# Kernel tuning notes

Hardware: AMD Instinct MI355X
Metric: run time of the kernel (lower is better)

Reference implementation:

```python
import jax, jax.numpy as jnp
import numpy as np

ALPHA = 0.4  # LeakyReLU negative slope used by the GAT


def _gat_head(h, W, a):
    # h: [N, F], W: [F, Fp], a: [2*Fp]; adjacency is all-ones so no masking
    Wh = h @ W                                   # [N, Fp]
    Fp = W.shape[1]
    e = jax.nn.leaky_relu(Wh @ a[:Fp][:, None] + (Wh @ a[Fp:])[None, :], ALPHA)
    att = jax.nn.softmax(e, axis=-1)             # [N, N]
    return att @ Wh                              # [N, Fp]


def _gat(h, W_heads, a_heads, W_gout, a_gout):
    # multi-head GAT: concat elu(head outputs), then single output attention layer
    heads = jax.vmap(_gat_head, in_axes=(None, 0, 0))(h, W_heads, a_heads)  # [H, N, Fp]
    x = jax.nn.elu(heads).transpose(1, 0, 2).reshape(h.shape[0], -1)        # [N, H*Fp]
    return jax.nn.elu(_gat_head(x, W_gout, a_gout))                          # [N, Cg]


def setup_inputs() -> dict:
    key = jax.random.key(0)
    ks = jax.random.split(key, 20)
    bs, R, S = 4, 512, 54
    h, w = 100, 152
    fc_dim, convs_dim4 = 1024, 512
    Cg, H, So = 256, 4, 128
    Fp = Cg // H
    sc = lambda k, shp, s=0.05: jax.random.normal(k, shp, dtype=jnp.float32) * s
    return {
        'region_f': jax.random.normal(ks[0], (bs * R, fc_dim), dtype=jnp.float32),
        'stuff_f': jax.random.normal(ks[1], (bs, convs_dim4, h, w), dtype=jnp.float32),
        'semseg_score': jax.random.normal(ks[2], (bs, S, h, w), dtype=jnp.float32),
        'W_rin': sc(ks[3], (fc_dim, Cg)), 'b_rin': jnp.zeros((Cg,), jnp.float32),
        'W_sin': sc(ks[4], (convs_dim4, Cg)), 'b_sin': jnp.zeros((Cg,), jnp.float32),
        'W_heads': sc(ks[5], (H, Cg, Fp), 0.1), 'a_heads': sc(ks[6], (H, 2 * Fp), 0.1),
        'W_gout': sc(ks[7], (H * Fp, Cg), 0.1), 'a_gout': sc(ks[8], (2 * Cg,), 0.1),
        'W_rout': sc(ks[9], (Cg, Cg)), 'b_rout': jnp.zeros((Cg,), jnp.float32),
        'W_sout': sc(ks[10], (Cg, So)), 'b_sout': jnp.zeros((So,), jnp.float32),
        'W_seg': sc(ks[11], (convs_dim4 + So, S)), 'b_seg': jnp.zeros((S,), jnp.float32),
    }


def reference(region_f, stuff_f, semseg_score,
              W_rin, b_rin, W_sin, b_sin,
              W_heads, a_heads, W_gout, a_gout,
              W_rout, b_rout, W_sout, b_sout,
              W_seg, b_seg):
    bs, Cd, h, w = stuff_f.shape
    S = semseg_score.shape[1]
    R = region_f.shape[0] // bs
    Cg = W_rin.shape[1]

    # node construction
    region_nodes = region_f @ W_rin + b_rin                           # [bs*R, Cg]
    score_flat = semseg_score.reshape(bs, S, h * w)
    class_center = jnp.einsum('bsn,bcn->bsc',
                              jax.nn.softmax(score_flat, axis=-1),
                              stuff_f.reshape(bs, Cd, h * w))          # [bs, S, Cd]
    class_nodes = class_center @ W_sin + b_sin                         # [bs, S, Cg]

    # per-image dense GAT over region + stuff nodes (batched via vmap)
    nodes = jnp.concatenate([region_nodes.reshape(bs, R, Cg), class_nodes], axis=1)
    graph_nodes = jax.vmap(lambda x: _gat(x, W_heads, a_heads, W_gout, a_gout))(nodes)
    new_region, new_class = graph_nodes[:, :R], graph_nodes[:, R:]

    # new box features: concat of original region features and projected graph features
    new_region_f = jnp.concatenate(
        [region_f, new_region.reshape(bs * R, Cg) @ W_rout + b_rout], axis=-1)

    # new stuff features: scatter class nodes back to pixels via class softmax
    new_class_nodes = new_class @ W_sout + b_sout                      # [bs, S, So]
    attn = jax.nn.softmax(score_flat, axis=1)                          # softmax over classes
    new_stuff = jnp.einsum('bsn,bso->bon', attn, new_class_nodes)      # [bs, So, h*w]
    new_stuff = new_stuff.reshape(bs, -1, h, w)

    # 1x1 conv seg head + x4 bilinear upsample (align_corners=False)
    seg_in = jnp.concatenate([stuff_f, new_stuff], axis=1)
    seg = jnp.einsum('bchw,co->bohw', seg_in, W_seg) + b_seg[None, :, None, None]
    segments = jax.image.resize(seg, (bs, S, 4 * h, 4 * w), method='bilinear')
    return new_region_f, segments
```

## Files before the change

kernel.cpp:

```cpp
#include <hip/hip_runtime.h>

#define HW 15200
#define SSD 54
#define NBATCH 4
#define NNODE 566
#define NPAD 576
#define CGD 256
#define CDD 512
#define NSPLIT 25
#define KSPAN 608

typedef __attribute__((ext_vector_type(4))) float f32x4;
typedef __attribute__((ext_vector_type(8))) short bf16x8;
typedef unsigned short ushort_t;

#define BT_RIN   0
#define BT_SIN   262144
#define BT_HEADS 393216
#define BT_GOUT  458752
#define BT_ROUT  524288
#define BT_SOUT  589824
#define BT_SEG2  622592
#define BT_TOTAL 630784

static constexpr long OFF_P     = 0;
static constexpr long OFF_CC    = OFF_P     + (long)NBATCH*SSD*HW;
static constexpr long OFF_NODES = OFF_CC    + (long)NBATCH*64*CDD;
static constexpr long OFF_WH    = OFF_NODES + (long)NBATCH*NNODE*CGD;
static constexpr long OFF_S1    = OFF_WH    + (long)16*NNODE*64;
static constexpr long OFF_S2    = OFF_S1    + 16*NPAD;
static constexpr long OFF_X     = OFF_S2    + 16*NPAD;
static constexpr long OFF_WH2   = OFF_X     + (long)NBATCH*NNODE*CGD;
static constexpr long OFF_S1B   = OFF_WH2   + (long)NBATCH*NNODE*CGD;
static constexpr long OFF_S2B   = OFF_S1B   + NBATCH*NPAD;
static constexpr long OFF_G     = OFF_S2B   + NBATCH*NPAD;
static constexpr long OFF_SUMS  = OFF_G     + (long)NBATCH*NNODE*CGD;
static constexpr long OFF_BT    = OFF_SUMS  + 256;
static constexpr long OFF_ASEG  = OFF_BT    + (BT_TOTAL/2 + 8);
static constexpr long OFF_SEG   = OFF_ASEG  + (long)NBATCH*64*576/2;
static constexpr long OFF_RFB   = OFF_SEG   + (long)NBATCH*SSD*HW;
static constexpr long OFF_WCOMB = OFF_RFB   + 1048576;
static constexpr long OFF_B2    = OFF_WCOMB + 8192;
static constexpr long OFF_ATTNB = OFF_B2    + 64;

__device__ inline float lrelu04(float x){ return x >= 0.f ? x : 0.4f*x; }
__device__ inline float eluf(float x){ return x > 0.f ? x : __expf(x) - 1.f; }
__device__ inline ushort_t f2bf(float f){
    unsigned u = __float_as_uint(f);
    return (ushort_t)((u + 0x7FFFu + ((u >> 16) & 1u)) >> 16);
}
__device__ inline float bf2f(ushort_t u){ return __uint_as_float((unsigned)u << 16); }
__device__ inline bf16x8 pack8(float4 lo, float4 hi){
    union { bf16x8 v; ushort_t u[8]; } p;
    p.u[0]=f2bf(lo.x); p.u[1]=f2bf(lo.y); p.u[2]=f2bf(lo.z); p.u[3]=f2bf(lo.w);
    p.u[4]=f2bf(hi.x); p.u[5]=f2bf(hi.y); p.u[6]=f2bf(hi.z); p.u[7]=f2bf(hi.w);
    return p.v;
}

__global__ __launch_bounds__(512)
void softmax_p(const float* __restrict__ score, ushort_t* __restrict__ pb,
               float* __restrict__ sums, float* __restrict__ s1s2b_zero,
               float* __restrict__ ccp)
{
    int blk = blockIdx.x;
    int t = threadIdx.x;
    if (blk < 256) {
        int b = blk >> 6, s = blk & 63;
        ushort_t* prow = pb + ((long)b*64 + s)*HW;
        if (s >= SSD) {
            for (int i = t; i < HW; i += 512) prow[i] = 0;
            if (t == 0) sums[b*64 + s] = 1.f;
            return;
        }
        const float* row = score + ((long)b*SSD + s)*HW;
        __shared__ float red[8];
        float s_ = 0.f;
        for (int i = t; i < HW; i += 512) {
            float e = __expf(row[i]);
            s_ += e;
            prow[i] = f2bf(e);
        }
        #pragma unroll
        for (int off = 32; off >= 1; off >>= 1) s_ += __shfl_down(s_, off);
        if ((t & 63) == 0) red[t >> 6] = s_;
        __syncthreads();
        if (t == 0) {
            float tot = 0.f;
            #pragma unroll
            for (int u = 0; u < 8; ++u) tot += red[u];
            sums[b*64 + s] = tot;
        }
        return;
    }
    long gid = (long)(blk - 256)*512 + t;
    if (gid < 4608) { s1s2b_zero[gid] = 0.f; return; }
    gid -= 4608;
    if (gid < (long)NBATCH*64*CDD) ccp[gid] = 0.f;
}

__global__ __launch_bounds__(256)
void cc_prep(const ushort_t* __restrict__ pb, const float* __restrict__ stuff,
             ushort_t* __restrict__ sbout, float* __restrict__ ccp,
             const float* __restrict__ score, ushort_t* __restrict__ attnb,
             const float* __restrict__ rf, float* __restrict__ out_region,
             ushort_t* __restrict__ rfb,
             const float* __restrict__ W_seg, ushort_t* __restrict__ asegb,
             const float* __restrict__ W_rin, const float* __restrict__ W_sin,
             const float* __restrict__ W_heads, const float* __restrict__ W_gout,
             const float* __restrict__ W_rout, const float* __restrict__ W_sout,
             const float* __restrict__ b_sout,
             ushort_t* __restrict__ bt, ushort_t* __restrict__ wcomb,
             float* __restrict__ bias2)
{
    int bid = blockIdx.x;
    if (bid < 832) {
        int g = (bid >> 6) * 8 + (bid & 7);
        if (g >= NSPLIT*NBATCH) return;
        int nt = (bid >> 3) & 7;
        int ks = g >> 2, b = g & 3;

        int w = threadIdx.x >> 6, l = threadIdx.x & 63;
        int lr = l & 15, lk = l >> 4;
        int n0 = nt*64 + w*16;
        const ushort_t* Prow = pb + ((long)b*64 + lr)*HW;
        const float*    Srow = stuff + ((long)b*CDD + n0 + lr)*HW;
        ushort_t*       Sout = sbout + ((long)b*CDD + n0 + lr)*HW;
        f32x4 acc[4] = {};
        int kbeg = ks * KSPAN;
        for (int k0 = kbeg; k0 < kbeg + KSPAN; k0 += 32) {
            int kk = k0 + lk*8;
            float4 lo = *(const float4*)&Srow[kk];
            float4 hi = *(const float4*)&Srow[kk + 4];
            bf16x8 bfv = pack8(lo, hi);
            *(bf16x8*)&Sout[kk] = bfv;
            #pragma unroll
            for (int mi = 0; mi < 4; ++mi) {
                bf16x8 af = *(const bf16x8*)&Prow[(long)mi*16*HW + kk];
                acc[mi] = __builtin_amdgcn_mfma_f32_16x16x32_bf16(af, bfv, acc[mi], 0, 0, 0);
            }
        }
        int c = n0 + lr;
        #pragma unroll
        for (int mi = 0; mi < 4; ++mi)
            #pragma unroll
            for (int r = 0; r < 4; ++r) {
                int m = mi*16 + lk*4 + r;
                atomicAdd(&ccp[((long)b*64 + m)*CDD + c], acc[mi][r]);
            }
        return;
    }
    long gid = (long)(bid - 832) * 256 + threadIdx.x;
    if (gid < (long)NBATCH*HW) {
        int b = (int)(gid / HW), n = (int)(gid % HW);
        const float* sp = score + (long)b*SSD*HW + n;
        float v[SSD];
        float m = -1e30f;
        #pragma unroll
        for (int s = 0; s < SSD; ++s) { v[s] = sp[(long)s*HW]; m = fmaxf(m, v[s]); }
        float sum = 0.f;
        #pragma unroll
        for (int s = 0; s < SSD; ++s) { v[s] = __expf(v[s] - m); sum += v[s]; }
        float inv = 1.f / sum;
        ushort_t* ap = attnb + (long)b*64*HW + n;
        #pragma unroll
        for (int s = 0; s < SSD; ++s) ap[(long)s*HW] = f2bf(v[s] * inv);
        #pragma unroll
        for (int s = SSD; s < 64; ++s) ap[(long)s*HW] = 0;
        return;
    }
    gid -= (long)NBATCH*HW;
    if (gid < 524288) {
        long row = gid / 256, col = gid % 256;
        float4 v = reinterpret_cast<const float4*>(rf)[gid];
        reinterpret_cast<float4*>(out_region)[row*320 + col] = v;
        union { ushort_t u[4]; uint2 q; } pk;
        pk.u[0]=f2bf(v.x); pk.u[1]=f2bf(v.y); pk.u[2]=f2bf(v.z); pk.u[3]=f2bf(v.w);
        reinterpret_cast<uint2*>(rfb)[gid] = pk.q;
        return;
    }
    gid -= 524288;
    if (gid < 131072) {
        int b = (int)(gid >> 15);
        int r = (int)(gid & 32767);
        int o = r >> 9, k = r & 511;
        asegb[(long)b*36864 + (long)o*576 + k] = f2bf(o < SSD ? W_seg[k*SSD + o] : 0.f);
        return;
    }
    gid -= 131072;
    if (gid < BT_TOTAL) {
        int i = (int)gid;
        float v;
        if (i < BT_SIN)        { int j=i;            int n=j>>10, k=j&1023; v = W_rin[k*256+n]; }
        else if (i < BT_HEADS) { int j=i-BT_SIN;     int n=j>>9,  k=j&511;  v = W_sin[k*256+n]; }
        else if (i < BT_GOUT)  { int j=i-BT_HEADS;   int h=j>>14, r=j&16383; int f=r>>8, k=r&255;
                                 v = W_heads[(h*256+k)*64+f]; }
        else if (i < BT_ROUT)  { int j=i-BT_GOUT;    int n=j>>8,  k=j&255;  v = W_gout[k*256+n]; }
        else if (i < BT_SOUT)  { int j=i-BT_ROUT;    int n=j>>8,  k=j&255;  v = W_rout[k*256+n]; }
        else if (i < BT_SEG2)  { int j=i-BT_SOUT;    int n=j>>8,  k=j&255;  v = W_sout[k*128+n]; }
        else                   { int j=i-BT_SEG2;    int o=j>>7,  k=j&127;
                                 v = (o < SSD) ? W_seg[(512+k)*SSD + o] : 0.f; }
        bt[i] = f2bf(v);
        return;
    }
    gid -= BT_TOTAL;
    if (gid < 16384) {
        int od = (int)(gid >> 8), k = (int)(gid & 255);
        float v = 0.f;
        if (od < SSD)
            for (int o = 0; o < 128; ++o)
                v += W_sout[k*128 + o] * W_seg[(512+o)*SSD + od];
        wcomb[(long)od*256 + k] = f2bf(v);
        return;
    }
    gid -= 16384;
    if (gid < 64) {
        int od = (int)gid;
        float v = 0.f;
        if (od < SSD)
            for (int o = 0; o < 128; ++o)
                v += b_sout[o] * W_seg[(512+o)*SSD + od];
        bias2[od] = v;
    }
}

__device__ __forceinline__
void seg512_body(int nt, int b,
                 const ushort_t* __restrict__ stuffb,
                 const ushort_t* __restrict__ asegb, const float* __restrict__ b_seg,
                 float* __restrict__ seg)
{
    int w = threadIdx.x >> 6, l = threadIdx.x & 63;
    int lr = l & 15, lk = l >> 4;
    int n0 = nt*128 + w*32;
    const ushort_t* A = asegb + (long)b*36864;
    const ushort_t* S = stuffb + (long)b*CDD*HW;
    f32x4 acc[4][2] = {};
    int n1 = min(n0 + lr, HW-1);
    int n2 = min(n0 + 16 + lr, HW-1);

    for (int k0 = 0; k0 < 512; k0 += 32) {
        const ushort_t* Bsrc = S + (long)k0*HW;
        long kb = (long)(lk*8)*HW;
        union { bf16x8 v; ushort_t u[8]; } b0, b1;
        #pragma unroll
        for (int u = 0; u < 8; ++u) {
            b0.u[u] = Bsrc[kb + (long)u*HW + n1];
            b1.u[u] = Bsrc[kb + (long)u*HW + n2];
        }
        #pragma unroll
        for (int ot = 0; ot < 4; ++ot) {
            bf16x8 af = *(const bf16x8*)&A[(ot*16 + lr)*576 + k0 + lk*8];
            acc[ot][0] = __builtin_amdgcn_mfma_f32_16x16x32_bf16(af, b0.v, acc[ot][0], 0,0,0);
            acc[ot][1] = __builtin_amdgcn_mfma_f32_16x16x32_bf16(af, b1.v, acc[ot][1], 0,0,0);
        }
    }

    #pragma unroll
    for (int ot = 0; ot < 4; ++ot) {
        #pragma unroll
        for (int r = 0; r < 4; ++r) {
            int o = ot*16 + lk*4 + r;
            if (o >= SSD) continue;
            float bb = b_seg[o];
            int na = n0 + lr, nb = n0 + 16 + lr;
            if (na < HW) seg[((long)b*SSD + o)*HW + na] = acc[ot][0][r] + bb;
            if (nb < HW) seg[((long)b*SSD + o)*HW + nb] = acc[ot][1][r] + bb;
        }
    }
}

__device__ __forceinline__
void segk64_body(int nt, int b,
                 const ushort_t* __restrict__ attnb,
                 const ushort_t* __restrict__ asegb,
                 float* __restrict__ seg)
{
    int w = threadIdx.x >> 6, l = threadIdx.x & 63;
    int lr = l & 15, lk = l >> 4;
    int n0 = nt*128 + w*32;
    const ushort_t* A = asegb + (long)b*36864;
    const ushort_t* T = attnb + (long)b*64*HW;
    f32x4 acc[4][2] = {};
    int n1 = min(n0 + lr, HW-1);
    int n2 = min(n0 + 16 + lr, HW-1);

    #pragma unroll
    for (int k0 = 512; k0 < 576; k0 += 32) {
        const ushort_t* Bsrc = T + (long)(k0-512)*HW;
        long kb = (long)(lk*8)*HW;
        union { bf16x8 v; ushort_t u[8]; } b0, b1;
        #pragma unroll
        for (int u = 0; u < 8; ++u) {
            b0.u[u] = Bsrc[kb + (long)u*HW + n1];
            b1.u[u] = Bsrc[kb + (long)u*HW + n2];
        }
        #pragma unroll
        for (int ot = 0; ot < 4; ++ot) {
            bf16x8 af = *(const bf16x8*)&A[(ot*16 + lr)*576 + k0 + lk*8];
            acc[ot][0] = __builtin_amdgcn_mfma_f32_16x16x32_bf16(af, b0.v, acc[ot][0], 0,0,0);
            acc[ot][1] = __builtin_amdgcn_mfma_f32_16x16x32_bf16(af, b1.v, acc[ot][1], 0,0,0);
        }
    }

    #pragma unroll
    for (int ot = 0; ot < 4; ++ot) {
        #pragma unroll
        for (int r = 0; r < 4; ++r) {
            int o = ot*16 + lk*4 + r;
            if (o >= SSD) continue;
            int na = n0 + lr, nb = n0 + 16 + lr;
            if (na < HW) { long i = ((long)b*SSD + o)*HW + na; seg[i] += acc[ot][0][r]; }
            if (nb < HW) { long i = ((long)b*SSD + o)*HW + nb; seg[i] += acc[ot][1][r]; }
        }
    }
}

template<bool AF32, int OUTMODE>
__device__ __forceinline__
void mm_body(int bx, int by, int bz,
             const void* __restrict__ Ap, const ushort_t* __restrict__ Bt,
             void* __restrict__ Cp, const float* __restrict__ bias,
             int M, int N, int K, int lda, int ldc,
             long sA, int zdivA, long sB, int zmodB, long sC)
{
    int z = bz;
    int w = threadIdx.x >> 6, l = threadIdx.x & 63;
    int lr = l & 15, lk = l >> 4;
    int m0 = bx * 64 + w * 16;
    int n0 = by * 64;
    const ushort_t* bt = Bt + (long)(z % zmodB) * sB;
    int mload = min(m0 + lr, M - 1);
    const float*    Af = (const float*)Ap    + (long)(z / zdivA) * sA + (long)mload * lda;
    const ushort_t* Ab = (const ushort_t*)Ap + (long)(z / zdivA) * sA + (long)mload * lda;
    f32x4 acc[4] = {};

    #pragma unroll 2
    for (int k0 = 0; k0 < K; k0 += 32) {
        int kk = k0 + lk * 8;
        bf16x8 af;
        if (AF32) {
            float4 lo = *(const float4*)&Af[kk];
            float4 hi = *(const float4*)&Af[kk + 4];
            af = pack8(lo, hi);
        } else {
            af = *(const bf16x8*)&Ab[kk];
        }
        #pragma unroll
        for (int j = 0; j < 4; ++j) {
            bf16x8 bf = *(const bf16x8*)&bt[(long)(n0 + j*16 + lr) * K + kk];
            acc[j] = __builtin_amdgcn_mfma_f32_16x16x32_bf16(af, bf, acc[j], 0, 0, 0);
        }
    }

    #pragma unroll
    for (int j = 0; j < 4; ++j) {
        int n = n0 + j*16 + lr;
        float bb = bias ? bias[n] : 0.f;
        #pragma unroll
        for (int r = 0; r < 4; ++r) {
            int m = m0 + lk*4 + r;
            if (OUTMODE == 2) {
                float v = acc[j][r] + bb;
                ((ushort_t*)Cp)[(long)z * sC + (long)n * ldc + m] =
                    (m < M) ? f2bf(v) : (ushort_t)0;
            } else {
                if (m >= M) continue;
                float v = acc[j][r] + bb;
                if (OUTMODE == 0)
                    ((float*)Cp)[(long)z * sC + (long)m * ldc + n] = v;
                else
                    ((ushort_t*)Cp)[(long)z * sC + (long)m * ldc + n] = f2bf(v);
            }
        }
    }
}

__global__ __launch_bounds__(256)
void nodes_seg(const ushort_t* __restrict__ rfb, const ushort_t* __restrict__ btRin,
               const float* __restrict__ ccp, const float* __restrict__ sums,
               const ushort_t* __restrict__ btSin, ushort_t* __restrict__ nodes,
               const float* __restrict__ b_rin, const float* __restrict__ b_sin,
               const ushort_t* __restrict__ stuffb, const ushort_t* __restrict__ asegb,
               const float* __restrict__ b_seg, float* __restrict__ segb)
{
    int bid = blockIdx.x;
    if (bid >= 144) {
        int sid = bid - 144;
        seg512_body(sid % 119, sid / 119, stuffb, asegb, b_seg, segb);
        return;
    }
    int bx = bid % 9, by = (bid/9) % 4, bz = bid / 36;
    if (bx < 8) {
        mm_body<false, 1>(bx, by, bz, rfb, btRin, nodes, b_rin,
                          512, 256, 1024, 1024, 256, 512L*1024, 1, 0, 1, (long)NNODE*CGD);
        return;
    }
    int w = threadIdx.x >> 6, l = threadIdx.x & 63;
    int lr = l & 15, lk = l >> 4;
    int m0 = w * 16, n0 = by * 64;
    int mload = min(m0 + lr, SSD - 1);
    const float* Af = ccp + ((long)bz*64 + mload)*CDD;
    float inv = 1.f / sums[bz*64 + mload];
    f32x4 acc[4] = {};

    #pragma unroll 2
    for (int k0 = 0; k0 < CDD; k0 += 32) {
        int kk = k0 + lk * 8;
        float4 lo = *(const float4*)&Af[kk];
        float4 hi = *(const float4*)&Af[kk + 4];
        lo.x *= inv; lo.y *= inv; lo.z *= inv; lo.w *= inv;
        hi.x *= inv; hi.y *= inv; hi.z *= inv; hi.w *= inv;
        bf16x8 af = pack8(lo, hi);
        #pragma unroll
        for (int j = 0; j < 4; ++j) {
            bf16x8 bf = *(const bf16x8*)&btSin[(long)(n0 + j*16 + lr) * CDD + kk];
            acc[j] = __builtin_amdgcn_mfma_f32_16x16x32_bf16(af, bf, acc[j], 0, 0, 0);
        }
    }

    #pragma unroll
    for (int j = 0; j < 4; ++j) {
        int n = n0 + j*16 + lr;
        float bb = b_sin[n];
        #pragma unroll
        for (int r = 0; r < 4; ++r) {
            int m = m0 + lk*4 + r;
            if (m >= SSD) continue;
            nodes[(long)bz*NNODE*CGD + (long)(512 + m)*CGD + n] = f2bf(acc[j][r] + bb);
        }
    }
}

__global__ __launch_bounds__(256)
void wht_seg(const ushort_t* __restrict__ nodes, const ushort_t* __restrict__ btHeads,
             ushort_t* __restrict__ wht, const float* __restrict__ a_heads,
             float* __restrict__ s1, float* __restrict__ s2,
             const ushort_t* __restrict__ stuffb, const ushort_t* __restrict__ asegb,
             const float* __restrict__ b_seg, float* __restrict__ segb)
{
    int bid = blockIdx.x;
    if (bid >= 144) {
        int sid = bid - 144 + 80;
        seg512_body(sid % 119, sid / 119, stuffb, asegb, b_seg, segb);
        return;
    }
    int bx = bid % 9, z = bid / 9;
    int w = threadIdx.x >> 6, l = threadIdx.x & 63;
    int lr = l & 15, lk = l >> 4;
    int m0 = bx*64 + w*16;
    const ushort_t* bt = btHeads + (long)(z & 3) * (64L*256);
    int mload = min(m0 + lr, NNODE - 1);
    const ushort_t* Ab = nodes + (long)(z >> 2)*((long)NNODE*CGD) + (long)mload*CGD;
    f32x4 acc[4] = {};

    #pragma unroll 2
    for (int k0 = 0; k0 < 256; k0 += 32) {
        int kk = k0 + lk*8;
        bf16x8 af = *(const bf16x8*)&Ab[kk];
        #pragma unroll
        for (int j = 0; j < 4; ++j) {
            bf16x8 bf = *(const bf16x8*)&bt[(long)(j*16 + lr)*256 + kk];
            acc[j] = __builtin_amdgcn_mfma_f32_16x16x32_bf16(af, bf, acc[j], 0, 0, 0);
        }
    }

    const float* av = a_heads + (long)(z & 3)*128;
    ushort_t* Wout = wht + (long)z*(64L*NPAD);
    float p1[4] = {0.f,0.f,0.f,0.f}, p2[4] = {0.f,0.f,0.f,0.f};
    #pragma unroll
    for (int j = 0; j < 4; ++j) {
        int f = j*16 + lr;
        float c1 = av[f], c2 = av[64 + f];
        #pragma unroll
        for (int r = 0; r < 4; ++r) {
            int m = m0 + lk*4 + r;
            float v = acc[j][r];
            Wout[(long)f*NPAD + m] = (m < NNODE) ? f2bf(v) : (ushort_t)0;
            if (m < NNODE) { p1[r] += v*c1; p2[r] += v*c2; }
        }
    }
    #pragma unroll
    for (int r = 0; r < 4; ++r)
        #pragma unroll
        for (int off = 1; off < 16; off <<= 1) {
            p1[r] += __shfl_xor(p1[r], off);
            p2[r] += __shfl_xor(p2[r], off);
        }
    if (lr == 0) {
        #pragma unroll
        for (int r = 0; r < 4; ++r) {
            int m = m0 + lk*4 + r;
            if (m < NNODE) {
                s1[(long)z*NPAD + m] = p1[r];
                s2[(long)z*NPAD + m] = p2[r];
            }
        }
    }
}

template<int F, int HEADMODE>
__device__ __forceinline__
void att_body(int bx, int z, const ushort_t* __restrict__ WhTall,
              const float* __restrict__ s1v, const float* __restrict__ s2v,
              ushort_t* __restrict__ outbuf)
{
    constexpr int FT = F / 16;
    const ushort_t* W  = WhTall + (long)z * F * NPAD;
    const float* s1 = s1v + (long)z * NPAD;
    const float* s2 = s2v + (long)z * NPAD;
    int w = threadIdx.x >> 6, l = threadIdx.x & 63;
    int lr = l & 15, lk = l >> 4;

    __shared__ float s2sh[NPAD];
    __shared__ float redm[4];
    float mxl = -1e30f;
    for (int i = threadIdx.x; i < NPAD; i += 256) {
        float v = (i < NNODE) ? s2[i] : -1e30f;
        s2sh[i] = v;
        mxl = fmaxf(mxl, v);
    }
    #pragma unroll
    for (int off = 32; off >= 1; off >>= 1) mxl = fmaxf(mxl, __shfl_down(mxl, off));
    if (l == 0) redm[w] = mxl;
    __syncthreads();
    float s2max = fmaxf(fmaxf(redm[0], redm[1]), fmaxf(redm[2], redm[3]));

    int m0 = bx * 64 + w * 16;
    float s1r = s1[min(m0 + lr, NNODE - 1)];
    float mrow = lrelu04(s1r + s2max);

    union { bf16x8 v; ushort_t u[8]; } onesu;
    #pragma unroll
    for (int u = 0; u < 8; ++u) onesu.u[u] = 0x3F80;
    bf16x8 ones = onesu.v;

    f32x4 acc[FT] = {};
    f32x4 accw = {};

    for (int j0 = 0; j0 < NPAD; j0 += 32) {
        float wv[8];
        #pragma unroll
        for (int u = 0; u < 8; ++u) {
            float e = lrelu04(s1r + s2sh[j0 + lk*8 + u]);
            wv[u] = __expf(e - mrow);
        }
        float4 lo = {wv[0], wv[1], wv[2], wv[3]};
        float4 hi = {wv[4], wv[5], wv[6], wv[7]};
        bf16x8 af = pack8(lo, hi);
        accw = __builtin_amdgcn_mfma_f32_16x16x32_bf16(af, ones, accw, 0, 0, 0);
        #pragma unroll
        for (int ft = 0; ft < FT; ++ft) {
            bf16x8 bf = *(const bf16x8*)&W[(long)(ft*16 + lr)*NPAD + j0 + lk*8];
            acc[ft] = __builtin_amdgcn_mfma_f32_16x16x32_bf16(af, bf, acc[ft], 0, 0, 0);
        }
    }

    #pragma unroll
    for (int r = 0; r < 4; ++r) {
        int m = m0 + lk*4 + r;
        if (m >= NNODE) continue;
        float inv = 1.f / accw[r];
        #pragma unroll
        for (int ft = 0; ft < FT; ++ft) {
            int f = ft*16 + lr;
            float v = eluf(acc[ft][r] * inv);
            if (HEADMODE) {
                int b = z >> 2, h = z & 3;
                outbuf[((long)(b*NNODE + m))*CGD + h*64 + f] = f2bf(v);
            } else {
                outbuf[((long)(z*NNODE + m))*CGD + f] = f2bf(v);
            }
        }
    }
}

__global__ __launch_bounds__(256)
void att64_seg(const ushort_t* __restrict__ wht, const float* __restrict__ s1,
               const float* __restrict__ s2, ushort_t* __restrict__ xbuf,
               const ushort_t* __restrict__ stuffb, const ushort_t* __restrict__ asegb,
               const float* __restrict__ b_seg, float* __restrict__ segb)
{
    int bid = blockIdx.x;
    if (bid >= 144) {
        int sid = bid - 144 + 160;
        seg512_body(sid % 119, sid / 119, stuffb, asegb, b_seg, segb);
        return;
    }
    att_body<64, 1>(bid % 9, bid / 9, wht, s1, s2, xbuf);
}

__global__ __launch_bounds__(256)
void wht2_seg(const ushort_t* __restrict__ xbuf, const ushort_t* __restrict__ btGout,
              ushort_t* __restrict__ wht2, const float* __restrict__ a_gout,
              float* __restrict__ s1b, float* __restrict__ s2b,
              const ushort_t* __restrict__ stuffb, const ushort_t* __restrict__ asegb,
              const float* __restrict__ b_seg, float* __restrict__ segb)
{
    int bid = blockIdx.x;
    if (bid >= 144) {
        int sid = bid - 144 + 240;
        seg512_body(sid % 119, sid / 119, stuffb, asegb, b_seg, segb);
        return;
    }
    int bx = bid % 9, by = (bid/9) % 4, z = bid / 36;
    int w = threadIdx.x >> 6, l = threadIdx.x & 63;
    int lr = l & 15, lk = l >> 4;
    int m0 = bx*64 + w*16;
    int n0 = by*64;
    int mload = min(m0 + lr, NNODE - 1);
    const ushort_t* Ab = xbuf + (long)z*((long)NNODE*CGD) + (long)mload*CGD;
    f32x4 acc[4] = {};

    #pragma unroll 2
    for (int k0 = 0; k0 < 256; k0 += 32) {
        int kk = k0 + lk*8;
        bf16x8 af = *(const bf16x8*)&Ab[kk];
        #pragma unroll
        for (int j = 0; j < 4; ++j) {
            bf16x8 bf = *(const bf16x8*)&btGout[(long)(n0 + j*16 + lr)*256 + kk];
            acc[j] = __builtin_amdgcn_mfma_f32_16x16x32_bf16(af, bf, acc[j], 0, 0, 0);
        }
    }

    ushort_t* Wout = wht2 + (long)z*(256L*NPAD);
    float p1[4] = {0.f,0.f,0.f,0.f}, p2[4] = {0.f,0.f,0.f,0.f};
    #pragma unroll
    for (int j = 0; j < 4; ++j) {
        int f = n0 + j*16 + lr;
        float c1 = a_gout[f], c2 = a_gout[256 + f];
        #pragma unroll
        for (int r = 0; r < 4; ++r) {
            int m = m0 + lk*4 + r;
            float v = acc[j][r];
            Wout[(long)f*NPAD + m] = (m < NNODE) ? f2bf(v) : (ushort_t)0;
            if (m < NNODE) { p1[r] += v*c1; p2[r] += v*c2; }
        }
    }
    #pragma unroll
    for (int r = 0; r < 4; ++r)
        #pragma unroll
        for (int off = 1; off < 16; off <<= 1) {
            p1[r] += __shfl_xor(p1[r], off);
            p2[r] += __shfl_xor(p2[r], off);
        }
    if (lr == 0) {
        #pragma unroll
        for (int r = 0; r < 4; ++r) {
            int m = m0 + lk*4 + r;
            if (m < NNODE) {
                atomicAdd(&s1b[(long)z*NPAD + m], p1[r]);
                atomicAdd(&s2b[(long)z*NPAD + m], p2[r]);
            }
        }
    }
}

__global__ __launch_bounds__(256)
void attg_seg(const ushort_t* __restrict__ wht2, const float* __restrict__ s1v,
              const float* __restrict__ s2v, ushort_t* __restrict__ g,
              const ushort_t* __restrict__ wcomb, const float* __restrict__ bias2,
              ushort_t* __restrict__ asegm2,
              const ushort_t* __restrict__ stuffb, const ushort_t* __restrict__ asegb,
              const float* __restrict__ b_seg, float* __restrict__ segb)
{
    int bid = blockIdx.x;
    if (bid >= 36) {
        int sid = bid - 36 + 320;
        seg512_body(sid % 119, sid / 119, stuffb, asegb, b_seg, segb);
        return;
    }
    int bx = bid % 9, z = bid / 9;
    const ushort_t* W  = wht2 + (long)z * (256L*NPAD);
    const float* s1 = s1v + (long)z * NPAD;
    const float* s2 = s2v + (long)z * NPAD;
    int t = threadIdx.x;
    int w = t >> 6, l = t & 63;
    int lr = l & 15, lk = l >> 4;

    __shared__ float s2sh[NPAD];
    __shared__ float redm[4];
    __shared__ ushort_t gld[64][264];

    float mxl = -1e30f;
    for (int i = t; i < NPAD; i += 256) {
        float v = (i < NNODE) ? s2[i] : -1e30f;
        s2sh[i] = v;
        mxl = fmaxf(mxl, v);
    }
    if (bx == 8)
        for (int i = t; i < 10*264; i += 256) gld[54 + i/264][i%264] = 0;
    #pragma unroll
    for (int off = 32; off >= 1; off >>= 1) mxl = fmaxf(mxl, __shfl_down(mxl, off));
    if (l == 0) redm[w] = mxl;
    __syncthreads();
    float s2max = fmaxf(fmaxf(redm[0], redm[1]), fmaxf(redm[2], redm[3]));

    int m0 = bx * 64 + w * 16;
    float s1r = s1[min(m0 + lr, NNODE - 1)];
    float mrow = lrelu04(s1r + s2max);

    union { bf16x8 v; ushort_t u[8]; } onesu;
    #pragma unroll
    for (int u = 0; u < 8; ++u) onesu.u[u] = 0x3F80;
    bf16x8 ones = onesu.v;

    f32x4 acc[16] = {};
    f32x4 accw = {};

    for (int j0 = 0; j0 < NPAD; j0 += 32) {
        float wv[8];
        #pragma unroll
        for (int u = 0; u < 8; ++u) {
            float e = lrelu04(s1r + s2sh[j0 + lk*8 + u]);
            wv[u] = __expf(e - mrow);
        }
        float4 lo = {wv[0], wv[1], wv[2], wv[3]};
        float4 hi = {wv[4], wv[5], wv[6], wv[7]};
        bf16x8 af = pack8(lo, hi);
        accw = __builtin_amdgcn_mfma_f32_16x16x32_bf16(af, ones, accw, 0, 0, 0);
        #pragma unroll
        for (int ft = 0; ft < 16; ++ft) {
            bf16x8 bf = *(const bf16x8*)&W[(long)(ft*16 + lr)*NPAD + j0 + lk*8];
            acc[ft] = __builtin_amdgcn_mfma_f32_16x16x32_bf16(af, bf, acc[ft], 0, 0, 0);
        }
    }

    #pragma unroll
    for (int r = 0; r < 4; ++r) {
        int m = m0 + lk*4 + r;
        if (m >= NNODE) continue;
        float inv = 1.f / accw[r];
        #pragma unroll
        for (int ft = 0; ft < 16; ++ft) {
            int f = ft*16 + lr;
            ushort_t vb = f2bf(eluf(acc[ft][r] * inv));
            g[((long)(z*NNODE + m))*CGD + f] = vb;
            if (bx == 8) gld[m - 512][f] = vb;
        }
    }

    if (bx == 8) {
        __syncthreads();
        f32x4 acc2[4] = {};
        #pragma unroll 2
        for (int k0 = 0; k0 < 256; k0 += 32) {
            int kk = k0 + lk*8;
            bf16x8 af = *(const bf16x8*)&gld[w*16 + lr][kk];
            #pragma unroll
            for (int j = 0; j < 4; ++j) {
                bf16x8 bf = *(const bf16x8*)&wcomb[(long)(j*16 + lr)*256 + kk];
                acc2[j] = __builtin_amdgcn_mfma_f32_16x16x32_bf16(af, bf, acc2[j], 0, 0, 0);
            }
        }
        #pragma unroll
        for (int j = 0; j < 4; ++j) {
            int n = j*16 + lr;
            float bb = bias2[n];
            #pragma unroll
            for (int r = 0; r < 4; ++r) {
                int m = w*16 + lk*4 + r;
                asegm2[(long)z*36864 + (long)n*576 + m] =
                    (m < SSD) ? f2bf(acc2[j][r] + bb) : (ushort_t)0;
            }
        }
    }
}

__global__ __launch_bounds__(256)
void rout_segk(const ushort_t* __restrict__ g_bf, const ushort_t* __restrict__ btRout,
               float* __restrict__ outreg, const float* __restrict__ b_rout,
               const ushort_t* __restrict__ attnb, const ushort_t* __restrict__ asegb,
               float* __restrict__ segb)
{
    int bid = blockIdx.x;
    if (bid < 128) {
        int x = bid & 7, y = (bid >> 3) & 3, z = bid >> 5;
        mm_body<false, 0>(x, y, z, g_bf, btRout, outreg, b_rout,
                          512, 256, 256, 256, 1280, (long)NNODE*CGD, 1, 0, 1, 512L*1280);
    } else {
        int sid = bid - 128;
        segk64_body(sid % 119, sid / 119, attnb, asegb, segb);
    }
}

__global__ __launch_bounds__(256)
void resize_v2_kernel(const float* __restrict__ seg, float* __restrict__ out)
{
    long u = (long)blockIdx.x * 256 + threadIdx.x;
    const long TOT4 = (long)NBATCH * SSD * 400 * 152;
    if (u >= TOT4) return;
    int m = (int)(u % 152);
    long r = u / 152;
    int y = (int)(r % 400);
    long c = r / 400;
    float fy = y * 0.25f - 0.375f;
    int y0 = (int)floorf(fy);
    float wy = fy - (float)y0;
    int y0c = max(y0, 0), y1c = min(y0 + 1, 99);
    const float* sp = seg + c * HW;
    int xm = max(m - 1, 0), xp = min(m + 1, 151);
    float r0a = sp[y0c * 152 + xm], r0b = sp[y0c * 152 + m], r0c = sp[y0c * 152 + xp];
    float r1a = sp[y1c * 152 + xm], r1b = sp[y1c * 152 + m], r1c = sp[y1c * 152 + xp];
    float ra = r0a + wy * (r1a - r0a);
    float rb = r0b + wy * (r1b - r0b);
    float rc = r0c + wy * (r1c - r0c);
    float4 o4;
    o4.x = 0.375f * ra + 0.625f * rb;
    o4.y = 0.125f * ra + 0.875f * rb;
    o4.z = 0.875f * rb + 0.125f * rc;
    o4.w = 0.625f * rb + 0.375f * rc;
    reinterpret_cast<float4*>(out)[u] = o4;
}

extern "C" void kernel_launch(void* const* d_in, const int* in_sizes, int n_in,
                              void* d_out, int out_size, void* d_ws, size_t ws_size,
                              hipStream_t stream)
{
    const float* region_f = (const float*)d_in[0];
    const float* stuff    = (const float*)d_in[1];
    const float* score    = (const float*)d_in[2];
    const float* W_rin    = (const float*)d_in[3];
    const float* b_rin    = (const float*)d_in[4];
    const float* W_sin    = (const float*)d_in[5];
    const float* b_sin    = (const float*)d_in[6];
    const float* W_heads  = (const float*)d_in[7];
    const float* a_heads  = (const float*)d_in[8];
    const float* W_gout   = (const float*)d_in[9];
    const float* a_gout   = (const float*)d_in[10];
    const float* W_rout   = (const float*)d_in[11];
    const float* b_rout   = (const float*)d_in[12];
    const float* W_sout   = (const float*)d_in[13];
    const float* b_sout   = (const float*)d_in[14];
    const float* W_seg    = (const float*)d_in[15];
    const float* b_seg    = (const float*)d_in[16];

    float* out = (float*)d_out;
    float* ws  = (float*)d_ws;

    ushort_t* pb   = (ushort_t*)(ws + OFF_P);
    float* ccp     = ws + OFF_CC;
    ushort_t* nodes_bf = (ushort_t*)(ws + OFF_NODES);
    ushort_t* wht  = (ushort_t*)(ws + OFF_WH);
    float* s1      = ws + OFF_S1;
    float* s2      = ws + OFF_S2;
    ushort_t* xbuf_bf = (ushort_t*)(ws + OFF_X);
    ushort_t* wht2 = (ushort_t*)(ws + OFF_WH2);
    float* s1b     = ws + OFF_S1B;
    float* s2b     = ws + OFF_S2B;
    ushort_t* g_bf = (ushort_t*)(ws + OFF_G);
    float* sums    = ws + OFF_SUMS;
    ushort_t* bt   = (ushort_t*)(ws + OFF_BT);
    ushort_t* asegb = (ushort_t*)(ws + OFF_ASEG);
    float* segb    = ws + OFF_SEG;
    ushort_t* rfb  = (ushort_t*)(ws + OFF_RFB);
    ushort_t* wcomb = (ushort_t*)(ws + OFF_WCOMB);
    float* bias2v  = ws + OFF_B2;
    ushort_t* attnb = (ushort_t*)(ws + OFF_ATTNB);

    float* out_region = out;
    float* out_seg    = out + 2048L*1280;
    ushort_t* stuffb  = (ushort_t*)out_seg;

    softmax_p<<<521, 512, 0, stream>>>(score, pb, sums, s1b, ccp);

    cc_prep<<<6158, 256, 0, stream>>>(pb, stuff, stuffb, ccp, score, attnb,
                                      region_f, out_region, rfb, W_seg, asegb,
                                      W_rin, W_sin, W_heads, W_gout, W_rout, W_sout,
                                      b_sout, bt, wcomb, bias2v);

    nodes_seg<<<224, 256, 0, stream>>>(
        rfb, bt + BT_RIN, ccp, sums, bt + BT_SIN, nodes_bf, b_rin, b_sin,
        stuffb, asegb, b_seg, segb);

    wht_seg<<<224, 256, 0, stream>>>(
        nodes_bf, bt + BT_HEADS, wht, a_heads, s1, s2,
        stuffb, asegb, b_seg, segb);

    att64_seg<<<224, 256, 0, stream>>>(
        wht, s1, s2, xbuf_bf, stuffb, asegb, b_seg, segb);

    wht2_seg<<<224, 256, 0, stream>>>(
        xbuf_bf, bt + BT_GOUT, wht2, a_gout, s1b, s2b,
        stuffb, asegb, b_seg, segb);

    attg_seg<<<192, 256, 0, stream>>>(
        wht2, s1b, s2b, g_bf, wcomb, bias2v, asegb + 512,
        stuffb, asegb, b_seg, segb);

    rout_segk<<<604, 256, 0, stream>>>(
        g_bf, bt + BT_ROUT, out_region + 1024, b_rout, attnb, asegb, segb);

    resize_v2_kernel<<<((long)NBATCH*SSD*400*152 + 255)/256, 256, 0, stream>>>(segb, out_seg);
}
```

Measured before the change: 282.7 us.

## Fuse score exponentiation and row sums into cc_prep, dropping softmax_p buffer

Removes the separate softmax_p kernel, which wrote exp(score) as a bf16 buffer plus row sums. cc_prep now computes exp(score) on the fly inside its MFMA loop and accumulates the row sums with atomics, and a small zero_init kernel clears the accumulators. This saves one full write and read of the intermediate buffer. In exchange, each fp32 score element is re-read and re-exponentiated by many waves, and padded class rows now keep a zero sum instead of one, which risks a divide-by-zero downstream.

```diff
diff --git a/kernel.cpp b/kernel.cpp
--- a/kernel.cpp
+++ b/kernel.cpp
@@ -57,50 +57,22 @@
     return p.v;
 }
 
-__global__ __launch_bounds__(512)
-void softmax_p(const float* __restrict__ score, ushort_t* __restrict__ pb,
-               float* __restrict__ sums, float* __restrict__ s1s2b_zero,
-               float* __restrict__ ccp)
-{
-    int blk = blockIdx.x;
-    int t = threadIdx.x;
-    if (blk < 256) {
-        int b = blk >> 6, s = blk & 63;
-        ushort_t* prow = pb + ((long)b*64 + s)*HW;
-        if (s >= SSD) {
-            for (int i = t; i < HW; i += 512) prow[i] = 0;
-            if (t == 0) sums[b*64 + s] = 1.f;
-            return;
-        }
-        const float* row = score + ((long)b*SSD + s)*HW;
-        __shared__ float red[8];
-        float s_ = 0.f;
-        for (int i = t; i < HW; i += 512) {
-            float e = __expf(row[i]);
-            s_ += e;
-            prow[i] = f2bf(e);
-        }
-        #pragma unroll
-        for (int off = 32; off >= 1; off >>= 1) s_ += __shfl_down(s_, off);
-        if ((t & 63) == 0) red[t >> 6] = s_;
-        __syncthreads();
-        if (t == 0) {
-            float tot = 0.f;
-            #pragma unroll
-            for (int u = 0; u < 8; ++u) tot += red[u];
-            sums[b*64 + s] = tot;
-        }
-        return;
-    }
-    long gid = (long)(blk - 256)*512 + t;
-    if (gid < 4608) { s1s2b_zero[gid] = 0.f; return; }
-    gid -= 4608;
-    if (gid < (long)NBATCH*64*CDD) ccp[gid] = 0.f;
-}
-
 __global__ __launch_bounds__(256)
-void cc_prep(const ushort_t* __restrict__ pb, const float* __restrict__ stuff,
+void zero_init(float* __restrict__ ccp, float* __restrict__ s1s2b,
+               float* __restrict__ sums)
+{
+    long i = (long)blockIdx.x*256 + threadIdx.x;
+    if (i < (long)NBATCH*64*CDD) { ccp[i] = 0.f; return; }
+    i -= (long)NBATCH*64*CDD;
+    if (i < 2L*NBATCH*NPAD) { s1s2b[i] = 0.f; return; }
+    i -= 2L*NBATCH*NPAD;
+    if (i < 256) sums[i] = 0.f;
+}
+
+__global__ __launch_bounds__(256)
+void cc_prep(const float* __restrict__ stuff,
              ushort_t* __restrict__ sbout, float* __restrict__ ccp,
+             float* __restrict__ sums,
              const float* __restrict__ score, ushort_t* __restrict__ attnb,
              const float* __restrict__ rf, float* __restrict__ out_region,
              ushort_t* __restrict__ rfb,
@@ -122,10 +94,10 @@
         int w = threadIdx.x >> 6, l = threadIdx.x & 63;
         int lr = l & 15, lk = l >> 4;
         int n0 = nt*64 + w*16;
-        const ushort_t* Prow = pb + ((long)b*64 + lr)*HW;
-        const float*    Srow = stuff + ((long)b*CDD + n0 + lr)*HW;
-        ushort_t*       Sout = sbout + ((long)b*CDD + n0 + lr)*HW;
+        const float* Srow = stuff + ((long)b*CDD + n0 + lr)*HW;
+        ushort_t*    Sout = sbout + ((long)b*CDD + n0 + lr)*HW;
         f32x4 acc[4] = {};
+        float rsum[4] = {0.f, 0.f, 0.f, 0.f};
         int kbeg = ks * KSPAN;
         for (int k0 = kbeg; k0 < kbeg + KSPAN; k0 += 32) {
             int kk = k0 + lk*8;
@@ -135,7 +107,19 @@
             *(bf16x8*)&Sout[kk] = bfv;
             #pragma unroll
             for (int mi = 0; mi < 4; ++mi) {
-                bf16x8 af = *(const bf16x8*)&Prow[(long)mi*16*HW + kk];
+                int s = lr + mi*16;
+                bf16x8 af = {};
+                if (s < SSD) {
+                    const float* sc = score + ((long)b*SSD + s)*HW + kk;
+                    float4 a0 = *(const float4*)sc;
+                    float4 a1 = *(const float4*)(sc + 4);
+                    a0.x = __expf(a0.x); a0.y = __expf(a0.y);
+                    a0.z = __expf(a0.z); a0.w = __expf(a0.w);
+                    a1.x = __expf(a1.x); a1.y = __expf(a1.y);
+                    a1.z = __expf(a1.z); a1.w = __expf(a1.w);
+                    rsum[mi] += a0.x + a0.y + a0.z + a0.w + a1.x + a1.y + a1.z + a1.w;
+                    af = pack8(a0, a1);
+                }
                 acc[mi] = __builtin_amdgcn_mfma_f32_16x16x32_bf16(af, bfv, acc[mi], 0, 0, 0);
             }
         }
@@ -147,6 +131,16 @@
                 int m = mi*16 + lk*4 + r;
                 atomicAdd(&ccp[((long)b*64 + m)*CDD + c], acc[mi][r]);
             }
+        if (nt == 0 && w == 0) {
+            #pragma unroll
+            for (int mi = 0; mi < 4; ++mi) {
+                float v = rsum[mi];
+                v += __shfl_down(v, 16);
+                v += __shfl_down(v, 32);
+                int s = lr + mi*16;
+                if (lk == 0 && s < SSD) atomicAdd(&sums[b*64 + s], v);
+            }
+        }
         return;
     }
     long gid = (long)(bid - 832) * 256 + threadIdx.x;
@@ -837,7 +831,6 @@
     float* out = (float*)d_out;
     float* ws  = (float*)d_ws;
 
-    ushort_t* pb   = (ushort_t*)(ws + OFF_P);
     float* ccp     = ws + OFF_CC;
     ushort_t* nodes_bf = (ushort_t*)(ws + OFF_NODES);
     ushort_t* wht  = (ushort_t*)(ws + OFF_WH);
@@ -861,9 +854,9 @@
     float* out_seg    = out + 2048L*1280;
     ushort_t* stuffb  = (ushort_t*)out_seg;
 
-    softmax_p<<<521, 512, 0, stream>>>(score, pb, sums, s1b, ccp);
-
-    cc_prep<<<6158, 256, 0, stream>>>(pb, stuff, stuffb, ccp, score, attnb,
+    zero_init<<<532, 256, 0, stream>>>(ccp, s1b, sums);
+
+    cc_prep<<<6158, 256, 0, stream>>>(stuff, stuffb, ccp, sums, score, attnb,
                                       region_f, out_region, rfb, W_seg, asegb,
                                       W_rin, W_sin, W_heads, W_gout, W_rout, W_sout,
                                       b_sout, bt, wcomb, bias2v);
```

New measurement: 280.9 us. Within noise of the previous version (-0.6%).

## Split fp32→bf16 stuff conversion from class-context GEMM and widen K-split

Applied to the files above, without the earlier changes.

The stuff-feature bf16 conversion now runs as an elementwise streaming pass inside a merged prep kernel, which also takes over the softmax, the zeroing and the weight prep. The class-context GEMM becomes a separate kernel that reads the bf16 copy, with the K-split raised from 25 to 95 chunks so far more blocks are in flight. The softmax loops are vectorised to float4 loads and 8-wide zero stores. In exchange, the stuff tensor is now read twice (once as fp32, once as bf16), and the wider split means more atomicAdd traffic on the accumulation buffer.

```diff
diff --git a/kernel.cpp b/kernel.cpp
--- a/kernel.cpp
+++ b/kernel.cpp
@@ -7,8 +7,10 @@
 #define NPAD 576
 #define CGD 256
 #define CDD 512
-#define NSPLIT 25
-#define KSPAN 608
+#define NSPLIT 95
+#define KSPAN 160
+#define NGRP (NSPLIT*NBATCH)
+#define CCBLK 3072
 
 typedef __attribute__((ext_vector_type(4))) float f32x4;
 typedef __attribute__((ext_vector_type(8))) short bf16x8;
@@ -57,10 +59,22 @@
     return p.v;
 }
 
-__global__ __launch_bounds__(512)
-void softmax_p(const float* __restrict__ score, ushort_t* __restrict__ pb,
-               float* __restrict__ sums, float* __restrict__ s1s2b_zero,
-               float* __restrict__ ccp)
+#define SB_GIDS 1945600L
+__global__ __launch_bounds__(256)
+void stream_prep(const float* __restrict__ score, ushort_t* __restrict__ pb,
+                 float* __restrict__ sums,
+                 const float* __restrict__ stuff, ushort_t* __restrict__ stuffb,
+                 ushort_t* __restrict__ attnb,
+                 const float* __restrict__ rf, float* __restrict__ out_region,
+                 ushort_t* __restrict__ rfb,
+                 const float* __restrict__ W_seg, ushort_t* __restrict__ asegb,
+                 const float* __restrict__ W_rin, const float* __restrict__ W_sin,
+                 const float* __restrict__ W_heads, const float* __restrict__ W_gout,
+                 const float* __restrict__ W_rout, const float* __restrict__ W_sout,
+                 const float* __restrict__ b_sout,
+                 ushort_t* __restrict__ bt, ushort_t* __restrict__ wcomb,
+                 float* __restrict__ bias2,
+                 float* __restrict__ ccp, float* __restrict__ s1s2b)
 {
     int blk = blockIdx.x;
     int t = threadIdx.x;
@@ -68,88 +82,44 @@
         int b = blk >> 6, s = blk & 63;
         ushort_t* prow = pb + ((long)b*64 + s)*HW;
         if (s >= SSD) {
-            for (int i = t; i < HW; i += 512) prow[i] = 0;
+            union { bf16x8 v; ushort_t u[8]; } z; 
+            #pragma unroll
+            for (int u = 0; u < 8; ++u) z.u[u] = 0;
+            for (int i = t*8; i < HW; i += 2048) *(bf16x8*)&prow[i] = z.v;
             if (t == 0) sums[b*64 + s] = 1.f;
             return;
         }
         const float* row = score + ((long)b*SSD + s)*HW;
-        __shared__ float red[8];
+        __shared__ float red[4];
         float s_ = 0.f;
-        for (int i = t; i < HW; i += 512) {
-            float e = __expf(row[i]);
-            s_ += e;
-            prow[i] = f2bf(e);
+        for (int i = t*4; i < HW; i += 1024) {
+            float4 x = *(const float4*)&row[i];
+            x.x = __expf(x.x); x.y = __expf(x.y);
+            x.z = __expf(x.z); x.w = __expf(x.w);
+            s_ += x.x + x.y + x.z + x.w;
+            union { ushort_t u[4]; uint2 q; } pk;
+            pk.u[0]=f2bf(x.x); pk.u[1]=f2bf(x.y); pk.u[2]=f2bf(x.z); pk.u[3]=f2bf(x.w);
+            *(uint2*)&prow[i] = pk.q;
         }
         #pragma unroll
         for (int off = 32; off >= 1; off >>= 1) s_ += __shfl_down(s_, off);
         if ((t & 63) == 0) red[t >> 6] = s_;
         __syncthreads();
-        if (t == 0) {
-            float tot = 0.f;
-            #pragma unroll
-            for (int u = 0; u < 8; ++u) tot += red[u];
-            sums[b*64 + s] = tot;
-        }
-        return;
-    }
-    long gid = (long)(blk - 256)*512 + t;
-    if (gid < 4608) { s1s2b_zero[gid] = 0.f; return; }
-    gid -= 4608;
-    if (gid < (long)NBATCH*64*CDD) ccp[gid] = 0.f;
-}
-
-__global__ __launch_bounds__(256)
-void cc_prep(const ushort_t* __restrict__ pb, const float* __restrict__ stuff,
-             ushort_t* __restrict__ sbout, float* __restrict__ ccp,
-             const float* __restrict__ score, ushort_t* __restrict__ attnb,
-             const float* __restrict__ rf, float* __restrict__ out_region,
-             ushort_t* __restrict__ rfb,
-             const float* __restrict__ W_seg, ushort_t* __restrict__ asegb,
-             const float* __restrict__ W_rin, const float* __restrict__ W_sin,
-             const float* __restrict__ W_heads, const float* __restrict__ W_gout,
-             const float* __restrict__ W_rout, const float* __restrict__ W_sout,
-             const float* __restrict__ b_sout,
-             ushort_t* __restrict__ bt, ushort_t* __restrict__ wcomb,
-             float* __restrict__ bias2)
-{
-    int bid = blockIdx.x;
-    if (bid < 832) {
-        int g = (bid >> 6) * 8 + (bid & 7);
-        if (g >= NSPLIT*NBATCH) return;
-        int nt = (bid >> 3) & 7;
-        int ks = g >> 2, b = g & 3;
-
-        int w = threadIdx.x >> 6, l = threadIdx.x & 63;
-        int lr = l & 15, lk = l >> 4;
-        int n0 = nt*64 + w*16;
-        const ushort_t* Prow = pb + ((long)b*64 + lr)*HW;
-        const float*    Srow = stuff + ((long)b*CDD + n0 + lr)*HW;
-        ushort_t*       Sout = sbout + ((long)b*CDD + n0 + lr)*HW;
-        f32x4 acc[4] = {};
-        int kbeg = ks * KSPAN;
-        for (int k0 = kbeg; k0 < kbeg + KSPAN; k0 += 32) {
-            int kk = k0 + lk*8;
-            float4 lo = *(const float4*)&Srow[kk];
-            float4 hi = *(const float4*)&Srow[kk + 4];
-            bf16x8 bfv = pack8(lo, hi);
-            *(bf16x8*)&Sout[kk] = bfv;
-            #pragma unroll
-            for (int mi = 0; mi < 4; ++mi) {
-                bf16x8 af = *(const bf16x8*)&Prow[(long)mi*16*HW + kk];
-                acc[mi] = __builtin_amdgcn_mfma_f32_16x16x32_bf16(af, bfv, acc[mi], 0, 0, 0);
-            }
-        }
-        int c = n0 + lr;
-        #pragma unroll
-        for (int mi = 0; mi < 4; ++mi)
-            #pragma unroll
-            for (int r = 0; r < 4; ++r) {
-                int m = mi*16 + lk*4 + r;
-                atomicAdd(&ccp[((long)b*64 + m)*CDD + c], acc[mi][r]);
-            }
-        return;
-    }
-    long gid = (long)(bid - 832) * 256 + threadIdx.x;
+        if (t == 0) sums[b*64 + s] = red[0] + red[1] + red[2] + red[3];
+        return;
+    }
+    long gid = (long)(blk - 256)*256 + t;
+    if (gid < SB_GIDS) {
+        long base = gid * 16;
+        float4 v0 = *(const float4*)&stuff[base];
+        float4 v1 = *(const float4*)&stuff[base + 4];
+        float4 v2 = *(const float4*)&stuff[base + 8];
+        float4 v3 = *(const float4*)&stuff[base + 12];
+        *(bf16x8*)&stuffb[base]     = pack8(v0, v1);
+        *(bf16x8*)&stuffb[base + 8] = pack8(v2, v3);
+        return;
+    }
+    gid -= SB_GIDS;
     if (gid < (long)NBATCH*HW) {
         int b = (int)(gid / HW), n = (int)(gid % HW);
         const float* sp = score + (long)b*SSD*HW + n;
@@ -220,7 +190,52 @@
             for (int o = 0; o < 128; ++o)
                 v += b_sout[o] * W_seg[(512+o)*SSD + od];
         bias2[od] = v;
-    }
+        return;
+    }
+    gid -= 64;
+    if (gid < 131072) { ccp[gid] = 0.f; return; }
+    gid -= 131072;
+    if (gid < 4608) s1s2b[gid] = 0.f;
+}
+
+__global__ __launch_bounds__(256)
+void cc_gemm(const ushort_t* __restrict__ pb, const ushort_t* __restrict__ stuffb,
+             float* __restrict__ ccp)
+{
+    int bid = blockIdx.x;
+    int g = (bid >> 6) * 8 + (bid & 7);
+    if (g >= NGRP) return;
+    int nt = (bid >> 3) & 7;
+    int ks = g >> 2, b = g & 3;
+
+    int w = threadIdx.x >> 6, l = threadIdx.x & 63;
+    int lr = l & 15, lk = l >> 4;
+    int n0 = nt*64 + w*16;
+    const ushort_t* Prow = pb + ((long)b*64 + lr)*HW;
+    const ushort_t* Srow = stuffb + ((long)b*CDD + n0 + lr)*HW;
+    f32x4 acc[4] = {};
+    int kbeg = ks * KSPAN;
+    #pragma unroll
+    for (int k0 = kbeg; k0 < kbeg + KSPAN; k0 += 32) {
+        int kk = k0 + lk*8;
+        bf16x8 sv = *(const bf16x8*)&Srow[kk];
+        bf16x8 p0 = *(const bf16x8*)&Prow[kk];
+        bf16x8 p1 = *(const bf16x8*)&Prow[(long)16*HW + kk];
+        bf16x8 p2 = *(const bf16x8*)&Prow[(long)32*HW + kk];
+        bf16x8 p3 = *(const bf16x8*)&Prow[(long)48*HW + kk];
+        acc[0] = __builtin_amdgcn_mfma_f32_16x16x32_bf16(p0, sv, acc[0], 0, 0, 0);
+        acc[1] = __builtin_amdgcn_mfma_f32_16x16x32_bf16(p1, sv, acc[1], 0, 0, 0);
+        acc[2] = __builtin_amdgcn_mfma_f32_16x16x32_bf16(p2, sv, acc[2], 0, 0, 0);
+        acc[3] = __builtin_amdgcn_mfma_f32_16x16x32_bf16(p3, sv, acc[3], 0, 0, 0);
+    }
+    int c = n0 + lr;
+    #pragma unroll
+    for (int mi = 0; mi < 4; ++mi)
+        #pragma unroll
+        for (int r = 0; r < 4; ++r) {
+            int m = mi*16 + lk*4 + r;
+            atomicAdd(&ccp[((long)b*64 + m)*CDD + c], acc[mi][r]);
+        }
 }
 
 __device__ __forceinline__
@@ -861,12 +876,12 @@
     float* out_seg    = out + 2048L*1280;
     ushort_t* stuffb  = (ushort_t*)out_seg;
 
-    softmax_p<<<521, 512, 0, stream>>>(score, pb, sums, s1b, ccp);
-
-    cc_prep<<<6158, 256, 0, stream>>>(pb, stuff, stuffb, ccp, score, attnb,
-                                      region_f, out_region, rfb, W_seg, asegb,
-                                      W_rin, W_sin, W_heads, W_gout, W_rout, W_sout,
-                                      b_sout, bt, wcomb, bias2v);
+    stream_prep<<<13712, 256, 0, stream>>>(score, pb, sums, stuff, stuffb, attnb,
+                                           region_f, out_region, rfb, W_seg, asegb,
+                                           W_rin, W_sin, W_heads, W_gout, W_rout, W_sout,
+                                           b_sout, bt, wcomb, bias2v, ccp, s1b);
+
+    cc_gemm<<<CCBLK, 256, 0, stream>>>(pb, stuffb, ccp);
 
     nodes_seg<<<224, 256, 0, stream>>>(
         rfb, bt + BT_RIN, ccp, sums, bt + BT_SIN, nodes_bf, b_rin, b_sin,
```

Measured after the change: 270.8 us. 4.2% less time.
